# Kernel optimization log

Measured on AMD Instinct MI355X. Metric: run time of the kernel, lower is better.

Reference implementation:

```python
import jax, jax.numpy as jnp
import numpy as np

HEADS = 4
DIM_HEAD = 64
QUERY_DIM = 512
CONTEXT_DIM = 512
INNER = HEADS * DIM_HEAD  # 256
SCALE = DIM_HEAD ** -0.5


def setup_inputs() -> dict:
    key = jax.random.key(0)
    ks = jax.random.split(key, 9)
    b, n, m = 4, 2048, 2048
    inp = {
        'x1': jax.random.normal(ks[0], (b, n, QUERY_DIM), jnp.float32),
        'x2': jax.random.normal(ks[1], (b, n, QUERY_DIM), jnp.float32),
        'context': jax.random.normal(ks[2], (b, m, CONTEXT_DIM), jnp.float32),
        # weights stored [in, out] (= torch weight.T)
        'Wq': jax.random.normal(ks[3], (QUERY_DIM, INNER), jnp.float32) * (QUERY_DIM ** -0.5),
        'Wq2': jax.random.normal(ks[4], (QUERY_DIM, INNER), jnp.float32) * (QUERY_DIM ** -0.5),
        'Wk': jax.random.normal(ks[5], (CONTEXT_DIM, INNER), jnp.float32) * (CONTEXT_DIM ** -0.5),
        'Wv': jax.random.normal(ks[6], (CONTEXT_DIM, INNER), jnp.float32) * (CONTEXT_DIM ** -0.5),
        'Wo': jax.random.normal(ks[7], (INNER, QUERY_DIM), jnp.float32) * (INNER ** -0.5),
        'bo': jax.random.normal(ks[8], (QUERY_DIM,), jnp.float32) * 0.01,
    }
    return inp


def _split_heads(t):
    # [b, n, h*d] -> [b, h, n, d]
    b, n, _ = t.shape
    return t.reshape(b, n, HEADS, DIM_HEAD).transpose(0, 2, 1, 3)


def reference(x1, x2, context, Wq, Wq2, Wk, Wv, Wo, bo):
    q = _split_heads(x1 @ Wq)
    q2 = _split_heads(x2 @ Wq2)
    k = _split_heads(context @ Wk)
    v = _split_heads(context @ Wv)
    sim = jnp.einsum('bhid,bhjd->bhij', q, k) * SCALE
    sim2 = jnp.einsum('bhid,bhjd->bhij', q2, k) * SCALE
    attn = 0.3 * jax.nn.softmax(sim, axis=-1) + 0.7 * jax.nn.softmax(sim2, axis=-1)
    out = jnp.einsum('bhij,bhjd->bhid', attn, v)  # [b, h, n, d]
    b, h, n, d = out.shape
    out = out.transpose(0, 2, 1, 3).reshape(b, n, h * d)
    return out @ Wo + bo
```

## Files before the change

kernel.cpp:

```cpp
#include <hip/hip_runtime.h>

typedef __attribute__((ext_vector_type(8))) short bf16x8;
typedef __attribute__((ext_vector_type(4))) float f32x4;
typedef unsigned short ushort_t;
typedef unsigned int uint_t;

__device__ __forceinline__ ushort_t f2bf(float f) {
    return __builtin_bit_cast(ushort_t, (__bf16)f);
}
__device__ __forceinline__ uint_t pack2(float a, float b) {
    return (uint_t)f2bf(a) | ((uint_t)f2bf(b) << 16);
}

#define LOG2E 1.4426950408889634f

#define WT_OFF   0
#define WOT_OFF  524288
#define QKV_OFF  655360
#define QKV_SZ   2097152
#define QKV_OFF_Z3 (3 * (size_t)QKV_SZ)
#define O_OFF    9043968

__global__ __launch_bounds__(256) void transpose_w(
    const float* __restrict__ Wq, const float* __restrict__ Wq2,
    const float* __restrict__ Wk, const float* __restrict__ Wv,
    const float* __restrict__ Wo, ushort_t* __restrict__ ws)
{
    __shared__ ushort_t lT[64][72];
    const int j = blockIdx.y;
    const int bx = blockIdx.x;
    const float* in;
    ushort_t* out;
    int C;
    if (j < 4) {
        in = (j == 0) ? Wq : (j == 1) ? Wq2 : (j == 2) ? Wk : Wv;
        out = ws + WT_OFF + (size_t)j * 131072; C = 256;
    } else {
        in = Wo; out = ws + WOT_OFF; C = 512;
    }
    const int R = 131072 / C;
    const int tc = C >> 6;
    const int r0 = (bx / tc) * 64, c0 = (bx % tc) * 64;
    const int t = threadIdx.x;
    const int ir = t >> 4, ic = (t & 15) * 4;
#pragma unroll
    for (int i = 0; i < 4; ++i) {
        const int r = ir + i * 16;
        float4 v = *(const float4*)(in + (size_t)(r0 + r) * C + c0 + ic);
        uint2 w; w.x = pack2(v.x, v.y); w.y = pack2(v.z, v.w);
        *(uint2*)&lT[r][ic] = w;
    }
    __syncthreads();
    const int oc = t >> 2, rr0 = (t & 3) * 16;
    ushort_t g[16];
#pragma unroll
    for (int k = 0; k < 16; ++k) g[k] = lT[rr0 + k][oc];
    ushort_t* op = out + (size_t)(c0 + oc) * R + r0 + rr0;
    *(uint4*)op = *(const uint4*)&g[0];
    *(uint4*)(op + 8) = *(const uint4*)&g[8];
}

#define PROJ_STAGE(K0, BUF) do {                                                     \
    _Pragma("unroll")                                                                \
    for (int it_ = 0; it_ < 8; ++it_) {                                              \
        const int cc_ = tid + it_ * 256;                                             \
        const int g_ = (cc_ ^ (cc_ >> 3)) & 7;                                       \
        const ushort_t* bp_ = Bt + (size_t)(cc_ >> 3) * 512 + (K0) + g_ * 8;         \
        __builtin_amdgcn_global_load_lds(                                            \
            (const __attribute__((address_space(1))) void*)bp_,                      \
            (__attribute__((address_space(3))) void*)&lB[BUF][cc_ * 8], 16, 0, 0);   \
    }                                                                                \
} while (0)

__global__ __launch_bounds__(256) void proj_gemm(
    const float* __restrict__ x1, const float* __restrict__ x2,
    const float* __restrict__ ctx, const ushort_t* __restrict__ Wt,
    ushort_t* __restrict__ QKV)
{
    __shared__ __align__(16) ushort_t lB[2][256 * 64];
    const int z = blockIdx.y;
    const float* A = (z == 0) ? x1 : (z == 1) ? x2 : ctx;
    const ushort_t* Bt = Wt + (size_t)z * 131072;
    const float sc = (z < 2) ? (0.125f * LOG2E) : 1.0f;
    const int tid = threadIdx.x;
    const int wave = tid >> 6, lane = tid & 63;
    const int quad = lane >> 4, l16 = lane & 15;
    const int l7 = l16 & 7;
    const size_t row0 = (size_t)blockIdx.x * 64;

    PROJ_STAGE(0, 0);

    const float* arow = A + (row0 + wave * 16 + l16) * 512 + quad * 8;
    float4 a[4];
    a[0] = *(const float4*)(arow);
    a[1] = *(const float4*)(arow + 4);
    a[2] = *(const float4*)(arow + 32);
    a[3] = *(const float4*)(arow + 36);

    f32x4 acc[16] = {};
    for (int k0 = 0; k0 < 512; k0 += 64) {
        const int pb = (k0 >> 6) & 1;
        __syncthreads();
        if (k0 + 64 < 512) PROJ_STAGE(k0 + 64, 1 - pb);
        float4 n[4] = {a[0], a[1], a[2], a[3]};
        if (k0 + 64 < 512) {
            n[0] = *(const float4*)(arow + k0 + 64);
            n[1] = *(const float4*)(arow + k0 + 68);
            n[2] = *(const float4*)(arow + k0 + 96);
            n[3] = *(const float4*)(arow + k0 + 100);
        }
        bf16x8 af[2];
#pragma unroll
        for (int ks = 0; ks < 2; ++ks) {
            uint4 aw;
            aw.x = pack2(a[2 * ks].x, a[2 * ks].y);
            aw.y = pack2(a[2 * ks].z, a[2 * ks].w);
            aw.z = pack2(a[2 * ks + 1].x, a[2 * ks + 1].y);
            aw.w = pack2(a[2 * ks + 1].z, a[2 * ks + 1].w);
            af[ks] = __builtin_bit_cast(bf16x8, aw);
        }
#pragma unroll
        for (int c = 0; c < 16; ++c) {
#pragma unroll
            for (int ks = 0; ks < 2; ++ks) {
                bf16x8 bfr = *(const bf16x8*)&lB[pb][(c * 16 + l16) * 64 +
                                                     (((ks * 4 + quad) ^ l7) << 3)];
                acc[c] = __builtin_amdgcn_mfma_f32_16x16x32_bf16(af[ks], bfr, acc[c], 0, 0, 0);
            }
        }
        a[0] = n[0]; a[1] = n[1]; a[2] = n[2]; a[3] = n[3];
    }

    if (z == 3) {
        const int b = (int)(row0 >> 11);
        const int tokl = ((int)row0 & 2047) + wave * 16 + quad * 4;
        ushort_t* Vt = QKV + QKV_OFF_Z3;
#pragma unroll
        for (int c = 0; c < 16; ++c) {
            const int col = c * 16 + l16;
            const int h = col >> 6, d = col & 63;
            uint2 w;
            w.x = pack2(acc[c][0], acc[c][1]);
            w.y = pack2(acc[c][2], acc[c][3]);
            *(uint2*)(Vt + ((size_t)((b * 4 + h) * 64 + d)) * 2048 + tokl) = w;
        }
    } else {
        ushort_t* C = QKV + (size_t)z * QKV_SZ;
#pragma unroll
        for (int c = 0; c < 16; ++c) {
            const int col = c * 16 + l16;
#pragma unroll
            for (int r = 0; r < 4; ++r)
                C[(row0 + wave * 16 + quad * 4 + r) * 256 + col] = f2bf(acc[c][r] * sc);
        }
    }
}

#define OUT_STAGE(K0, BUF) do {                                                      \
    _Pragma("unroll")                                                                \
    for (int it_ = 0; it_ < 4; ++it_) {                                              \
        const int cc_ = tid + it_ * 256;                                             \
        const int g_ = (cc_ ^ (cc_ >> 3)) & 7;                                       \
        const ushort_t* bp_ = Wot + (size_t)(col0 + (cc_ >> 3)) * 256 + (K0) + g_ * 8; \
        __builtin_amdgcn_global_load_lds(                                            \
            (const __attribute__((address_space(1))) void*)bp_,                      \
            (__attribute__((address_space(3))) void*)&lB[BUF][cc_ * 8], 16, 0, 0);   \
    }                                                                                \
} while (0)

__global__ __launch_bounds__(256) void out_gemm(
    const ushort_t* __restrict__ Op, const ushort_t* __restrict__ Wot,
    const float* __restrict__ bias, float* __restrict__ out)
{
    __shared__ __align__(16) ushort_t lB[2][128 * 64];
    const int tid = threadIdx.x;
    const int wave = tid >> 6, lane = tid & 63;
    const int quad = lane >> 4, l16 = lane & 15;
    const int l7 = l16 & 7;
    const size_t row0 = (size_t)blockIdx.x * 64;
    const int col0 = blockIdx.y * 128;

    OUT_STAGE(0, 0);
    const ushort_t* arow = Op + (row0 + wave * 16 + l16) * 256 + quad * 8;
    bf16x8 af0 = *(const bf16x8*)(arow);
    bf16x8 af1 = *(const bf16x8*)(arow + 32);

    f32x4 acc[8] = {};
    for (int k0 = 0; k0 < 256; k0 += 64) {
        const int pb = (k0 >> 6) & 1;
        __syncthreads();
        if (k0 + 64 < 256) OUT_STAGE(k0 + 64, 1 - pb);
        bf16x8 an0 = af0, an1 = af1;
        if (k0 + 64 < 256) {
            an0 = *(const bf16x8*)(arow + k0 + 64);
            an1 = *(const bf16x8*)(arow + k0 + 96);
        }
#pragma unroll
        for (int c = 0; c < 8; ++c) {
            bf16x8 b0 = *(const bf16x8*)&lB[pb][(c * 16 + l16) * 64 + ((quad ^ l7) << 3)];
            acc[c] = __builtin_amdgcn_mfma_f32_16x16x32_bf16(af0, b0, acc[c], 0, 0, 0);
            bf16x8 b1 = *(const bf16x8*)&lB[pb][(c * 16 + l16) * 64 + (((4 + quad) ^ l7) << 3)];
            acc[c] = __builtin_amdgcn_mfma_f32_16x16x32_bf16(af1, b1, acc[c], 0, 0, 0);
        }
        af0 = an0; af1 = an1;
    }
#pragma unroll
    for (int c = 0; c < 8; ++c) {
        const int col = col0 + c * 16 + l16;
        const float bv = bias[col];
#pragma unroll
        for (int r = 0; r < 4; ++r)
            out[(row0 + wave * 16 + quad * 4 + r) * 512 + col] = acc[c][r] + bv;
    }
}


#define ATTN_STAGE(MB, KDST, VDST) do {                                                 \
    _Pragma("unroll")                                                                   \
    for (int it_ = 0; it_ < 2; ++it_) {                                                 \
        const int cc_ = tid + it_ * 256;                                                \
        const int g_ = (cc_ ^ (cc_ >> 3)) & 7;                                          \
        const ushort_t* kp_ = Kb + (size_t)(tok0 + (MB) + (cc_ >> 3)) * 256 + in0 + g_ * 8; \
        __builtin_amdgcn_global_load_lds(                                               \
            (const __attribute__((address_space(1))) void*)kp_,                         \
            (__attribute__((address_space(3))) void*)&(KDST)[cc_ * 8], 16, 0, 0);       \
        const ushort_t* vp_ = Vt + (size_t)(bh64 + (cc_ >> 3)) * 2048 + (MB) + g_ * 8;  \
        __builtin_amdgcn_global_load_lds(                                               \
            (const __attribute__((address_space(1))) void*)vp_,                         \
            (__attribute__((address_space(3))) void*)&(VDST)[cc_ * 8], 16, 0, 0);       \
    }                                                                                   \
} while (0)

__global__ __launch_bounds__(256) void attn_fused(
    const ushort_t* __restrict__ Qb, const ushort_t* __restrict__ Q2b,
    const ushort_t* __restrict__ Kb, const ushort_t* __restrict__ Vt,
    ushort_t* __restrict__ Ob)
{
    __shared__ __align__(16) ushort_t lK[3][64 * 64];
    __shared__ __align__(16) ushort_t lV[3][64 * 64];
    __shared__ __align__(16) ushort_t lP[4][2][16 * 72];

    const int qt = blockIdx.x;
    const int bh = blockIdx.y;
    const int tid = threadIdx.x;
    const int wave = tid >> 6, lane = tid & 63;
    const int quad = lane >> 4, l16 = lane & 15;
    const int l7 = l16 & 7;
    const size_t tok0 = (size_t)(bh >> 2) * 2048;
    const int in0 = (bh & 3) * 64;
    const int bh64 = bh * 64;
    ushort_t* lPw0 = &lP[wave][0][0];
    ushort_t* lPw1 = &lP[wave][1][0];

    bf16x8 q1f[2], q2f[2];
    {
        const ushort_t* qr1 = Qb  + (tok0 + qt * 64 + wave * 16 + l16) * 256 + in0;
        const ushort_t* qr2 = Q2b + (tok0 + qt * 64 + wave * 16 + l16) * 256 + in0;
#pragma unroll
        for (int ks = 0; ks < 2; ++ks) {
            q1f[ks] = *(const bf16x8*)(qr1 + ks * 32 + quad * 8);
            q2f[ks] = *(const bf16x8*)(qr2 + ks * 32 + quad * 8);
        }
    }

    ushort_t* pKcur = &lK[0][0]; ushort_t* pVcur = &lV[0][0];
    ushort_t* pKpre = &lK[1][0]; ushort_t* pVpre = &lV[1][0];
    ushort_t* pKold = &lK[2][0]; ushort_t* pVold = &lV[2][0];

    ATTN_STAGE(0, pKcur, pVcur);

    f32x4 o1[4] = {}, o2[4] = {};
    bf16x8 pa1[2], pa2[2];
    float l1 = 0.f, l2 = 0.f;

    for (int i = 0; i < 32; ++i) {
        __syncthreads();
        if (i < 31) ATTN_STAGE((i + 1) * 64, pKpre, pVpre);

        f32x4 st1[4] = {}, st2[4] = {};
#pragma unroll
        for (int c = 0; c < 4; ++c) {
#pragma unroll
            for (int ks = 0; ks < 2; ++ks) {
                bf16x8 kf = *(const bf16x8*)&pKcur[(c * 16 + l16) * 64 +
                                                   ((((ks * 4 + quad) ^ l7) & 7) << 3)];
                st1[c] = __builtin_amdgcn_mfma_f32_16x16x32_bf16(kf, q1f[ks], st1[c], 0, 0, 0);
                st2[c] = __builtin_amdgcn_mfma_f32_16x16x32_bf16(kf, q2f[ks], st2[c], 0, 0, 0);
            }
        }

        if (i > 0) {
#pragma unroll
            for (int c = 0; c < 4; ++c) {
#pragma unroll
                for (int ks = 0; ks < 2; ++ks) {
                    bf16x8 vf = *(const bf16x8*)&pVold[(c * 16 + l16) * 64 +
                                                       ((((ks * 4 + quad) ^ l7) & 7) << 3)];
                    o1[c] = __builtin_amdgcn_mfma_f32_16x16x32_bf16(vf, pa1[ks], o1[c], 0, 0, 0);
                    o2[c] = __builtin_amdgcn_mfma_f32_16x16x32_bf16(vf, pa2[ks], o2[c], 0, 0, 0);
                }
            }
        }

#pragma unroll
        for (int c = 0; c < 4; ++c) {
            float p0 = __builtin_amdgcn_exp2f(st1[c][0]);
            float p1 = __builtin_amdgcn_exp2f(st1[c][1]);
            float p2 = __builtin_amdgcn_exp2f(st1[c][2]);
            float p3 = __builtin_amdgcn_exp2f(st1[c][3]);
            l1 += (p0 + p1) + (p2 + p3);
            uint2 w; w.x = pack2(p0, p1); w.y = pack2(p2, p3);
            *(uint2*)&lPw0[l16 * 72 + c * 16 + quad * 4] = w;
            float r0 = __builtin_amdgcn_exp2f(st2[c][0]);
            float r1 = __builtin_amdgcn_exp2f(st2[c][1]);
            float r2 = __builtin_amdgcn_exp2f(st2[c][2]);
            float r3 = __builtin_amdgcn_exp2f(st2[c][3]);
            l2 += (r0 + r1) + (r2 + r3);
            uint2 y; y.x = pack2(r0, r1); y.y = pack2(r2, r3);
            *(uint2*)&lPw1[l16 * 72 + c * 16 + quad * 4] = y;
        }
#pragma unroll
        for (int ks = 0; ks < 2; ++ks) {
            pa1[ks] = *(const bf16x8*)&lPw0[l16 * 72 + ks * 32 + quad * 8];
            pa2[ks] = *(const bf16x8*)&lPw1[l16 * 72 + ks * 32 + quad * 8];
        }

        ushort_t* tK = pKold; pKold = pKcur; pKcur = pKpre; pKpre = tK;
        ushort_t* tV = pVold; pVold = pVcur; pVcur = pVpre; pVpre = tV;
    }

#pragma unroll
    for (int c = 0; c < 4; ++c) {
#pragma unroll
        for (int ks = 0; ks < 2; ++ks) {
            bf16x8 vf = *(const bf16x8*)&pVold[(c * 16 + l16) * 64 +
                                               ((((ks * 4 + quad) ^ l7) & 7) << 3)];
            o1[c] = __builtin_amdgcn_mfma_f32_16x16x32_bf16(vf, pa1[ks], o1[c], 0, 0, 0);
            o2[c] = __builtin_amdgcn_mfma_f32_16x16x32_bf16(vf, pa2[ks], o2[c], 0, 0, 0);
        }
    }

    l1 += __shfl_xor(l1, 16, 64); l1 += __shfl_xor(l1, 32, 64);
    l2 += __shfl_xor(l2, 16, 64); l2 += __shfl_xor(l2, 32, 64);
    const float inv1 = 0.3f / l1, inv2 = 0.7f / l2;

    ushort_t* orow = Ob + (tok0 + qt * 64 + wave * 16 + l16) * 256 + in0;
#pragma unroll
    for (int c = 0; c < 4; ++c) {
        const float f0 = o1[c][0] * inv1 + o2[c][0] * inv2;
        const float f1 = o1[c][1] * inv1 + o2[c][1] * inv2;
        const float f2 = o1[c][2] * inv1 + o2[c][2] * inv2;
        const float f3 = o1[c][3] * inv1 + o2[c][3] * inv2;
        uint2 w; w.x = pack2(f0, f1); w.y = pack2(f2, f3);
        *(uint2*)(orow + c * 16 + quad * 4) = w;
    }
}

extern "C" void kernel_launch(void* const* d_in, const int* in_sizes, int n_in,
                              void* d_out, int out_size, void* d_ws, size_t ws_size,
                              hipStream_t stream)
{
    (void)in_sizes; (void)n_in; (void)out_size; (void)ws_size;
    const float* x1  = (const float*)d_in[0];
    const float* x2  = (const float*)d_in[1];
    const float* ctx = (const float*)d_in[2];
    const float* Wq  = (const float*)d_in[3];
    const float* Wq2 = (const float*)d_in[4];
    const float* Wk  = (const float*)d_in[5];
    const float* Wv  = (const float*)d_in[6];
    const float* Wo  = (const float*)d_in[7];
    const float* bo  = (const float*)d_in[8];
    ushort_t* ws  = (ushort_t*)d_ws;
    float* out = (float*)d_out;

    ushort_t* Wt  = ws + WT_OFF;
    ushort_t* Wot = ws + WOT_OFF;
    ushort_t* QKV = ws + QKV_OFF;
    ushort_t* Q   = QKV;
    ushort_t* Q2  = QKV + 1 * (size_t)QKV_SZ;
    ushort_t* Kp  = QKV + 2 * (size_t)QKV_SZ;
    ushort_t* Vt  = QKV + 3 * (size_t)QKV_SZ;
    ushort_t* Op  = ws + O_OFF;

    transpose_w<<<dim3(32, 5),  256, 0, stream>>>(Wq, Wq2, Wk, Wv, Wo, ws);
    proj_gemm  <<<dim3(128, 4), 256, 0, stream>>>(x1, x2, ctx, Wt, QKV);
    attn_fused <<<dim3(32, 16), 256, 0, stream>>>(Q, Q2, Kp, Vt, Op);
    out_gemm   <<<dim3(128, 4), 256, 0, stream>>>(Op, Wot, bo, out);
}
```

Baseline: 170.1 us.

## Hold V tile in registers to cut LDS to double buffering, add MFMA priority

The V fragments for the current tile are now loaded from LDS into registers right after the matmuls. The PV product in the next iteration reads those registers instead of a third LDS buffer, so K/V staging drops from triple to double buffering and LDS use falls. That can allow more resident blocks per CU. s_setprio raises wave priority around the MFMA section. The cost is 32 extra VGPRs per thread, which may reduce occupancy.

```diff
diff --git a/kernel.cpp b/kernel.cpp
--- a/kernel.cpp
+++ b/kernel.cpp
@@ -236,8 +236,8 @@
     const ushort_t* __restrict__ Kb, const ushort_t* __restrict__ Vt,
     ushort_t* __restrict__ Ob)
 {
-    __shared__ __align__(16) ushort_t lK[3][64 * 64];
-    __shared__ __align__(16) ushort_t lV[3][64 * 64];
+    __shared__ __align__(16) ushort_t lK[2][64 * 64];
+    __shared__ __align__(16) ushort_t lV[2][64 * 64];
     __shared__ __align__(16) ushort_t lP[4][2][16 * 72];
 
     const int qt = blockIdx.x;
@@ -263,44 +263,48 @@
         }
     }
 
-    ushort_t* pKcur = &lK[0][0]; ushort_t* pVcur = &lV[0][0];
-    ushort_t* pKpre = &lK[1][0]; ushort_t* pVpre = &lV[1][0];
-    ushort_t* pKold = &lK[2][0]; ushort_t* pVold = &lV[2][0];
-
-    ATTN_STAGE(0, pKcur, pVcur);
+    ATTN_STAGE(0, lK[0], lV[0]);
 
     f32x4 o1[4] = {}, o2[4] = {};
     bf16x8 pa1[2], pa2[2];
+    bf16x8 vr[4][2];
     float l1 = 0.f, l2 = 0.f;
 
     for (int i = 0; i < 32; ++i) {
+        const int cb = i & 1;
         __syncthreads();
-        if (i < 31) ATTN_STAGE((i + 1) * 64, pKpre, pVpre);
-
+        if (i < 31) ATTN_STAGE((i + 1) * 64, lK[cb ^ 1], lV[cb ^ 1]);
+
+        __builtin_amdgcn_s_setprio(1);
         f32x4 st1[4] = {}, st2[4] = {};
 #pragma unroll
         for (int c = 0; c < 4; ++c) {
 #pragma unroll
             for (int ks = 0; ks < 2; ++ks) {
-                bf16x8 kf = *(const bf16x8*)&pKcur[(c * 16 + l16) * 64 +
-                                                   ((((ks * 4 + quad) ^ l7) & 7) << 3)];
+                bf16x8 kf = *(const bf16x8*)&lK[cb][(c * 16 + l16) * 64 +
+                                                    ((((ks * 4 + quad) ^ l7) & 7) << 3)];
                 st1[c] = __builtin_amdgcn_mfma_f32_16x16x32_bf16(kf, q1f[ks], st1[c], 0, 0, 0);
                 st2[c] = __builtin_amdgcn_mfma_f32_16x16x32_bf16(kf, q2f[ks], st2[c], 0, 0, 0);
             }
         }
-
         if (i > 0) {
 #pragma unroll
             for (int c = 0; c < 4; ++c) {
 #pragma unroll
                 for (int ks = 0; ks < 2; ++ks) {
-                    bf16x8 vf = *(const bf16x8*)&pVold[(c * 16 + l16) * 64 +
-                                                       ((((ks * 4 + quad) ^ l7) & 7) << 3)];
-                    o1[c] = __builtin_amdgcn_mfma_f32_16x16x32_bf16(vf, pa1[ks], o1[c], 0, 0, 0);
-                    o2[c] = __builtin_amdgcn_mfma_f32_16x16x32_bf16(vf, pa2[ks], o2[c], 0, 0, 0);
+                    o1[c] = __builtin_amdgcn_mfma_f32_16x16x32_bf16(vr[c][ks], pa1[ks], o1[c], 0, 0, 0);
+                    o2[c] = __builtin_amdgcn_mfma_f32_16x16x32_bf16(vr[c][ks], pa2[ks], o2[c], 0, 0, 0);
                 }
             }
         }
+        __builtin_amdgcn_s_setprio(0);
+
+#pragma unroll
+        for (int c = 0; c < 4; ++c)
+#pragma unroll
+            for (int ks = 0; ks < 2; ++ks)
+                vr[c][ks] = *(const bf16x8*)&lV[cb][(c * 16 + l16) * 64 +
+                                                    ((((ks * 4 + quad) ^ l7) & 7) << 3)];
 
 #pragma unroll
         for (int c = 0; c < 4; ++c) {
@@ -324,19 +328,14 @@
             pa1[ks] = *(const bf16x8*)&lPw0[l16 * 72 + ks * 32 + quad * 8];
             pa2[ks] = *(const bf16x8*)&lPw1[l16 * 72 + ks * 32 + quad * 8];
         }
-
-        ushort_t* tK = pKold; pKold = pKcur; pKcur = pKpre; pKpre = tK;
-        ushort_t* tV = pVold; pVold = pVcur; pVcur = pVpre; pVpre = tV;
     }
 
 #pragma unroll
     for (int c = 0; c < 4; ++c) {
 #pragma unroll
         for (int ks = 0; ks < 2; ++ks) {
-            bf16x8 vf = *(const bf16x8*)&pVold[(c * 16 + l16) * 64 +
-                                               ((((ks * 4 + quad) ^ l7) & 7) << 3)];
-            o1[c] = __builtin_amdgcn_mfma_f32_16x16x32_bf16(vf, pa1[ks], o1[c], 0, 0, 0);
-            o2[c] = __builtin_amdgcn_mfma_f32_16x16x32_bf16(vf, pa2[ks], o2[c], 0, 0, 0);
+            o1[c] = __builtin_amdgcn_mfma_f32_16x16x32_bf16(vr[c][ks], pa1[ks], o1[c], 0, 0, 0);
+            o2[c] = __builtin_amdgcn_mfma_f32_16x16x32_bf16(vr[c][ks], pa2[ks], o2[c], 0, 0, 0);
         }
     }
 
```

New measurement: 178.2 us. 1.05x slower.
